# Kernel optimization log

Hardware: AMD Instinct MI355X
Metric: run time of the kernel (lower is better)

Reference implementation:

```python
import jax, jax.numpy as jnp
import numpy as np

B, N, D_H, D_K = 128, 4096, 512, 512
D_C = 3 * D_H
C_CLIP = 10.0


def _xavier(key, shape, gain=1.414):
    fan_in, fan_out = shape[0], shape[1]
    bound = gain * np.sqrt(6.0 / (fan_in + fan_out))
    return jax.random.uniform(key, shape, jnp.float32, -bound, bound)


def setup_inputs() -> dict:
    key = jax.random.key(0)
    k1, k2, k3, k4 = jax.random.split(key, 4)
    return {
        "h_c": jax.random.normal(k1, (B, 1, D_C), jnp.float32),
        "H": jax.random.normal(k2, (B, N, D_H), jnp.float32),
        "W_Q": _xavier(k3, (D_C, D_K)),
        "W_K": _xavier(k4, (D_H, D_K)),
    }


def reference(h_c, H, W_Q, W_K):
    sqrt_d_k = jnp.asarray(W_K.shape[-1], jnp.float32) ** 0.5
    Q = h_c @ W_Q                                # [B, 1, d_k]
    K = jnp.einsum('bnd,dk->bnk', H, W_K)        # [B, N, d_k]
    U = jnp.einsum('bqk,bnk->bqn', Q, K) / sqrt_d_k  # [B, 1, N]
    U = jnp.squeeze(U, axis=1)                   # [B, N]
    return jax.nn.softmax(C_CLIP * jnp.tanh(U), axis=-1)
```

## Files before the change

kernel.cpp:

```cpp
#include <hip/hip_runtime.h>
#include <hip/hip_bf16.h>


#define B_SZ   128
#define N_SZ   4096
#define D_H    512
#define D_K    512
#define D_C    1536
#define RSQRT_DK 0.04419417382415922f

__global__ __launch_bounds__(256) void qpart_kernel(
    const float* __restrict__ h_c, const float* __restrict__ W_Q,
    float* __restrict__ Qp) {
  const int bg = blockIdx.x;
  const int cc = blockIdx.y;
  const int t  = threadIdx.x;

  __shared__ float hc[8 * 192];
  for (int i = t; i < 8 * 192; i += 256) {
    int bi = i / 192, ci = i % 192;
    hc[i] = h_c[(size_t)(bg * 8 + bi) * D_C + cc * 192 + ci];
  }
  __syncthreads();

  float2 acc[8];
#pragma unroll
  for (int bi = 0; bi < 8; ++bi) { acc[bi].x = 0.f; acc[bi].y = 0.f; }

  const int k2 = 2 * t;
#pragma unroll 4
  for (int ci = 0; ci < 192; ++ci) {
    const float2 w = *reinterpret_cast<const float2*>(
        W_Q + (size_t)(cc * 192 + ci) * D_K + k2);
#pragma unroll
    for (int bi = 0; bi < 8; ++bi) {
      const float h = hc[bi * 192 + ci];
      acc[bi].x += h * w.x;
      acc[bi].y += h * w.y;
    }
  }

#pragma unroll
  for (int bi = 0; bi < 8; ++bi) {
    *reinterpret_cast<float2*>(
        Qp + ((size_t)cc * B_SZ + bg * 8 + bi) * D_K + k2) = acc[bi];
  }
}

__global__ __launch_bounds__(256) void vcomp_kernel(
    const float* __restrict__ Qp, const float* __restrict__ W_K,
    float* __restrict__ v) {
  const int b  = blockIdx.x;
  const int dc = blockIdx.y;
  const int t  = threadIdx.x;

  __shared__ float q[D_K];
  for (int i = t; i < D_K; i += 256) {
    float s = 0.f;
#pragma unroll
    for (int cc = 0; cc < 8; ++cc)
      s += Qp[((size_t)cc * B_SZ + b) * D_K + i];
    q[i] = s;
  }
  __syncthreads();

  const int wave = t >> 6, lane = t & 63;
  const float4 q0 = *reinterpret_cast<const float4*>(&q[lane * 8]);
  const float4 q1 = *reinterpret_cast<const float4*>(&q[lane * 8 + 4]);

#pragma unroll
  for (int j = 0; j < 4; ++j) {
    const int d = dc * 16 + wave * 4 + j;
    const float4* wp =
        reinterpret_cast<const float4*>(W_K + (size_t)d * D_K + lane * 8);
    const float4 w0 = wp[0], w1 = wp[1];
    float dot = q0.x * w0.x + q0.y * w0.y + q0.z * w0.z + q0.w * w0.w +
                q1.x * w1.x + q1.y * w1.y + q1.z * w1.z + q1.w * w1.w;
#pragma unroll
    for (int off = 32; off; off >>= 1) dot += __shfl_xor(dot, off, 64);
    if (lane == 0) v[(size_t)b * D_H + d] = dot;
  }
}

__global__ __launch_bounds__(256) void score_kernel(
    const float* __restrict__ H, const float* __restrict__ v,
    float* __restrict__ out) {
  const int t = threadIdx.x;
  const int wave = t >> 6, lane = t & 63;
  const size_t row0 = (size_t)blockIdx.x * 32 + wave * 8;
  const int b = (int)(row0 >> 12);

  const float4* vp =
      reinterpret_cast<const float4*>(v + (size_t)b * D_H + lane * 8);
  const float4 v0 = vp[0], v1 = vp[1];

#pragma unroll
  for (int r = 0; r < 8; ++r) {
    const size_t row = row0 + r;
    const float4* hp =
        reinterpret_cast<const float4*>(H + row * D_H + lane * 8);
    const float4 h0 = hp[0], h1 = hp[1];
    float dot = h0.x * v0.x + h0.y * v0.y + h0.z * v0.z + h0.w * v0.w +
                h1.x * v1.x + h1.y * v1.y + h1.z * v1.z + h1.w * v1.w;
#pragma unroll
    for (int off = 32; off; off >>= 1) dot += __shfl_xor(dot, off, 64);
    if (lane == 0) {
      const float u = dot * RSQRT_DK;
      out[row] = expf(10.0f * tanhf(u) - 10.0f);
    }
  }
}

__global__ __launch_bounds__(256) void norm_kernel(float* __restrict__ out) {
  const int b = blockIdx.x;
  const int t = threadIdx.x;
  float* p = out + (size_t)b * N_SZ;

  float4 x[4];
  float s = 0.f;
#pragma unroll
  for (int j = 0; j < 4; ++j) {
    x[j] = *reinterpret_cast<const float4*>(p + 4 * (t + 256 * j));
    s += x[j].x + x[j].y + x[j].z + x[j].w;
  }

  __shared__ float red[256];
  red[t] = s;
  __syncthreads();
  for (int off = 128; off; off >>= 1) {
    if (t < off) red[t] += red[t + off];
    __syncthreads();
  }
  const float inv = 1.0f / red[0];

#pragma unroll
  for (int j = 0; j < 4; ++j) {
    x[j].x *= inv; x[j].y *= inv; x[j].z *= inv; x[j].w *= inv;
    *reinterpret_cast<float4*>(p + 4 * (t + 256 * j)) = x[j];
  }
}

extern "C" void kernel_launch(void* const* d_in, const int* in_sizes, int n_in,
                              void* d_out, int out_size, void* d_ws,
                              size_t ws_size, hipStream_t stream) {
  const float* h_c = (const float*)d_in[0];
  const float* H   = (const float*)d_in[1];
  const float* W_Q = (const float*)d_in[2];
  const float* W_K = (const float*)d_in[3];

  float* out = (float*)d_out;
  float* Qp  = (float*)d_out;
  float* v   = (float*)d_ws;

  qpart_kernel<<<dim3(16, 8), 256, 0, stream>>>(h_c, W_Q, Qp);
  vcomp_kernel<<<dim3(128, 32), 256, 0, stream>>>(Qp, W_K, v);
  score_kernel<<<dim3(16384), 256, 0, stream>>>(H, v, out);
  norm_kernel<<<dim3(128), 256, 0, stream>>>(out);
}
```

Before: 229.7 us.

## Grid-stride score kernel with nontemporal H loads and transposed shuffle reduction

The score kernel now runs a persistent-style grid-stride loop over 8-row tasks on a smaller grid. It loads H with nontemporal hints, since the data is streamed once. It replaces eight separate full-wave butterfly reductions with a transposed reduce-scatter across shuffles, so lanes 0-7 write the eight results. The aim is fewer shuffle instructions and less cache pollution in this bandwidth-bound pass, at the cost of more register pressure and some select instructions.

```diff
diff --git a/kernel.cpp b/kernel.cpp
--- a/kernel.cpp
+++ b/kernel.cpp
@@ -8,6 +8,9 @@
 #define D_K    512
 #define D_C    1536
 #define RSQRT_DK 0.04419417382415922f
+#define SCORE_GRID 4096
+
+typedef float f32x4 __attribute__((ext_vector_type(4)));
 
 __global__ __launch_bounds__(256) void qpart_kernel(
     const float* __restrict__ h_c, const float* __restrict__ W_Q,
@@ -86,27 +89,55 @@
     const float* __restrict__ H, const float* __restrict__ v,
     float* __restrict__ out) {
   const int t = threadIdx.x;
-  const int wave = t >> 6, lane = t & 63;
-  const size_t row0 = (size_t)blockIdx.x * 32 + wave * 8;
-  const int b = (int)(row0 >> 12);
+  const int lane = t & 63;
+  const int wave_gid = blockIdx.x * 4 + (t >> 6);
+  const int total_waves = SCORE_GRID * 4;
+  const int n_tasks = B_SZ * N_SZ / 8;
 
-  const float4* vp =
-      reinterpret_cast<const float4*>(v + (size_t)b * D_H + lane * 8);
-  const float4 v0 = vp[0], v1 = vp[1];
+  for (int task = wave_gid; task < n_tasks; task += total_waves) {
+    const size_t row0 = (size_t)task * 8;
+    const int b = (int)(row0 >> 12);
 
+    const f32x4* vp =
+        reinterpret_cast<const f32x4*>(v + (size_t)b * D_H + lane * 8);
+    const f32x4 v0 = vp[0], v1 = vp[1];
+
+    float p[8];
 #pragma unroll
-  for (int r = 0; r < 8; ++r) {
-    const size_t row = row0 + r;
-    const float4* hp =
-        reinterpret_cast<const float4*>(H + row * D_H + lane * 8);
-    const float4 h0 = hp[0], h1 = hp[1];
-    float dot = h0.x * v0.x + h0.y * v0.y + h0.z * v0.z + h0.w * v0.w +
-                h1.x * v1.x + h1.y * v1.y + h1.z * v1.z + h1.w * v1.w;
+    for (int r = 0; r < 8; ++r) {
+      const f32x4* hp =
+          reinterpret_cast<const f32x4*>(H + (row0 + r) * D_H + lane * 8);
+      const f32x4 h0 = __builtin_nontemporal_load(hp);
+      const f32x4 h1 = __builtin_nontemporal_load(hp + 1);
+      const f32x4 m = h0 * v0 + h1 * v1;
+      p[r] = (m.x + m.y) + (m.z + m.w);
+    }
+
+    float q[4];
 #pragma unroll
-    for (int off = 32; off; off >>= 1) dot += __shfl_xor(dot, off, 64);
-    if (lane == 0) {
-      const float u = dot * RSQRT_DK;
-      out[row] = expf(10.0f * tanhf(u) - 10.0f);
+    for (int j = 0; j < 4; ++j) {
+      const float keep = (lane & 1) ? p[2 * j + 1] : p[2 * j];
+      const float send = (lane & 1) ? p[2 * j]     : p[2 * j + 1];
+      q[j] = keep + __shfl_xor(send, 1, 64);
+    }
+    float r2[2];
+#pragma unroll
+    for (int i = 0; i < 2; ++i) {
+      const float keep = (lane & 2) ? q[2 * i + 1] : q[2 * i];
+      const float send = (lane & 2) ? q[2 * i]     : q[2 * i + 1];
+      r2[i] = keep + __shfl_xor(send, 2, 64);
+    }
+    {
+      const float keep = (lane & 4) ? r2[1] : r2[0];
+      const float send = (lane & 4) ? r2[0] : r2[1];
+      float s = keep + __shfl_xor(send, 4, 64);
+      s += __shfl_xor(s, 8, 64);
+      s += __shfl_xor(s, 16, 64);
+      s += __shfl_xor(s, 32, 64);
+      if (lane < 8) {
+        const float u = s * RSQRT_DK;
+        out[row0 + lane] = expf(10.0f * tanhf(u) - 10.0f);
+      }
     }
   }
 }
@@ -154,6 +185,6 @@
 
   qpart_kernel<<<dim3(16, 8), 256, 0, stream>>>(h_c, W_Q, Qp);
   vcomp_kernel<<<dim3(128, 32), 256, 0, stream>>>(Qp, W_K, v);
-  score_kernel<<<dim3(16384), 256, 0, stream>>>(H, v, out);
+  score_kernel<<<dim3(SCORE_GRID), 256, 0, stream>>>(H, v, out);
   norm_kernel<<<dim3(128), 256, 0, stream>>>(out);
 }
```

Result: slower. 250.7 us (+9.1%).

## Split Q partial-sum reduction into its own kernel and reuse W_K rows across batches

Applied to the files above, without the earlier changes.

Moves the reduction of Q partial sums out of vcomp into a separate qsum kernel that writes the full Q to workspace. vcomp now keeps four W_K rows in registers and loops over 16 batches, so W_K is read once per batch group instead of once per batch and the 8-way Qp sum is no longer repeated 32 times per batch. The grid shrinks from 4096 to 256 blocks. In exchange it adds one kernel launch and a Q round trip through memory, and the small grid may leave compute units underused.

```diff
diff --git a/kernel.cpp b/kernel.cpp
--- a/kernel.cpp
+++ b/kernel.cpp
@@ -8,6 +8,8 @@
 #define D_K    512
 #define D_C    1536
 #define RSQRT_DK 0.04419417382415922f
+
+typedef float f32x4 __attribute__((ext_vector_type(4)));
 
 __global__ __launch_bounds__(256) void qpart_kernel(
     const float* __restrict__ h_c, const float* __restrict__ W_Q,
@@ -47,38 +49,56 @@
   }
 }
 
-__global__ __launch_bounds__(256) void vcomp_kernel(
-    const float* __restrict__ Qp, const float* __restrict__ W_K,
-    float* __restrict__ v) {
-  const int b  = blockIdx.x;
-  const int dc = blockIdx.y;
-  const int t  = threadIdx.x;
-
-  __shared__ float q[D_K];
-  for (int i = t; i < D_K; i += 256) {
+__global__ __launch_bounds__(256) void qsum_kernel(
+    const float* __restrict__ Qp, float* __restrict__ Q) {
+  const int b = blockIdx.x;
+  const int t = threadIdx.x;
+  for (int k = t; k < D_K; k += 256) {
     float s = 0.f;
 #pragma unroll
     for (int cc = 0; cc < 8; ++cc)
-      s += Qp[((size_t)cc * B_SZ + b) * D_K + i];
-    q[i] = s;
+      s += Qp[((size_t)cc * B_SZ + b) * D_K + k];
+    Q[(size_t)b * D_K + k] = s;
   }
-  __syncthreads();
+}
 
-  const int wave = t >> 6, lane = t & 63;
-  const float4 q0 = *reinterpret_cast<const float4*>(&q[lane * 8]);
-  const float4 q1 = *reinterpret_cast<const float4*>(&q[lane * 8 + 4]);
+__global__ __launch_bounds__(256) void vcomp_kernel(
+    const float* __restrict__ Q, const float* __restrict__ W_K,
+    float* __restrict__ v) {
+  const int dc = blockIdx.x;
+  const int bg = blockIdx.y;
+  const int wave = threadIdx.x >> 6, lane = threadIdx.x & 63;
+  const int d0 = dc * 16 + wave * 4;
 
+  f32x4 w[4][2];
 #pragma unroll
   for (int j = 0; j < 4; ++j) {
-    const int d = dc * 16 + wave * 4 + j;
-    const float4* wp =
-        reinterpret_cast<const float4*>(W_K + (size_t)d * D_K + lane * 8);
-    const float4 w0 = wp[0], w1 = wp[1];
-    float dot = q0.x * w0.x + q0.y * w0.y + q0.z * w0.z + q0.w * w0.w +
-                q1.x * w1.x + q1.y * w1.y + q1.z * w1.z + q1.w * w1.w;
+    const f32x4* wp =
+        reinterpret_cast<const f32x4*>(W_K + (size_t)(d0 + j) * D_K + lane * 8);
+    w[j][0] = wp[0]; w[j][1] = wp[1];
+  }
+
+#pragma unroll 2
+  for (int bi = 0; bi < 16; ++bi) {
+    const int b = bg * 16 + bi;
+    const f32x4* qp =
+        reinterpret_cast<const f32x4*>(Q + (size_t)b * D_K + lane * 8);
+    const f32x4 q0 = qp[0], q1 = qp[1];
+    float dot[4];
 #pragma unroll
-    for (int off = 32; off; off >>= 1) dot += __shfl_xor(dot, off, 64);
-    if (lane == 0) v[(size_t)b * D_H + d] = dot;
+    for (int j = 0; j < 4; ++j) {
+      const f32x4 m = q0 * w[j][0] + q1 * w[j][1];
+      dot[j] = (m.x + m.y) + (m.z + m.w);
+    }
+#pragma unroll
+    for (int j = 0; j < 4; ++j) {
+#pragma unroll
+      for (int off = 32; off; off >>= 1) dot[j] += __shfl_xor(dot[j], off, 64);
+    }
+    if (lane == 0) {
+#pragma unroll
+      for (int j = 0; j < 4; ++j) v[(size_t)b * D_H + d0 + j] = dot[j];
+    }
   }
 }
 
@@ -150,10 +170,12 @@
 
   float* out = (float*)d_out;
   float* Qp  = (float*)d_out;
-  float* v   = (float*)d_ws;
+  float* Q   = (float*)d_ws;
+  float* v   = (float*)d_ws + B_SZ * D_K;
 
   qpart_kernel<<<dim3(16, 8), 256, 0, stream>>>(h_c, W_Q, Qp);
-  vcomp_kernel<<<dim3(128, 32), 256, 0, stream>>>(Qp, W_K, v);
+  qsum_kernel<<<dim3(128), 256, 0, stream>>>(Qp, Q);
+  vcomp_kernel<<<dim3(32, 8), 256, 0, stream>>>(Q, W_K, v);
   score_kernel<<<dim3(16384), 256, 0, stream>>>(H, v, out);
   norm_kernel<<<dim3(128), 256, 0, stream>>>(out);
 }
```

Result: no change. 231.1 us (+0.6%).
